# Kernel optimization log

Hardware: AMD Instinct MI355X
Metric: run time of the kernel (lower is better)

Reference implementation:

```python
import jax, jax.numpy as jnp
import numpy as np

B, K, S, L, H, A = 32, 128, 48, 2, 128, 500
NEG_INF = jnp.float32(-1e30)  # stand-in for -inf that is safe under fp16/bf16 too


def _gather_beam(x, idx):
    # x: (B, K, ...); idx: (B, K) -> x gathered along beam dim
    idx_b = idx.reshape(idx.shape + (1,) * (x.ndim - 2))
    return jnp.take_along_axis(x, jnp.broadcast_to(idx_b, idx.shape + x.shape[2:]), axis=1)


def setup_inputs() -> dict:
    key = jax.random.key(0)
    ks = jax.random.split(key, 12)
    return {
        "gen_ll": jax.random.normal(ks[0], (B, K), jnp.float32),
        "disc_ll": jax.random.normal(ks[1], (B, K), jnp.float32),
        "hiddens": jax.random.normal(ks[2], (B, K, S, L, H), jnp.float32),
        "cells": jax.random.normal(ks[3], (B, K, S, L, H), jnp.float32),
        "trees": jax.random.normal(ks[4], (B, K, S, H), jnp.float32),
        "beam_widths": jax.random.randint(ks[5], (B,), 1, K + 1, jnp.int64),
        "ncons_nts": jax.random.randint(ks[6], (B, K), 0, 8, jnp.int64),
        "nopen_parens": jax.random.randint(ks[7], (B, K), 0, 16, jnp.int64),
        "actions": jax.random.randint(ks[8], (B, K, A), 0, 30, jnp.int64),
        "actions_pos": jax.random.randint(ks[9], (B, K), 0, A, jnp.int64),
        "pointer": jax.random.randint(ks[10], (B, K), 0, S, jnp.int64),
        "size": 64,
    }


def reference(gen_ll, disc_ll, hiddens, cells, trees, beam_widths, ncons_nts,
              nopen_parens, actions, actions_pos, pointer, size):
    # BeamItems.shrink: mask beams outside active width, sort by score (desc),
    # gather all beam-indexed state by the sort permutation, clamp widths.
    beam_order = jnp.arange(K, dtype=beam_widths.dtype)          # (K,)
    outside = beam_order[None, :] >= beam_widths[:, None]        # (B, K)
    masked = jnp.where(outside, NEG_INF, gen_ll)                 # (B, K)

    sort_idx = jnp.argsort(-masked, axis=1)                      # descending
    gen_sorted = jnp.take_along_axis(masked, sort_idx, axis=1)

    disc_sorted = jnp.take_along_axis(disc_ll, sort_idx, axis=1)
    hiddens_s = _gather_beam(hiddens, sort_idx)
    cells_s = _gather_beam(cells, sort_idx)
    trees_s = _gather_beam(trees, sort_idx)
    ncons_s = jnp.take_along_axis(ncons_nts, sort_idx, axis=1)
    nopen_s = jnp.take_along_axis(nopen_parens, sort_idx, axis=1)
    actions_s = _gather_beam(actions, sort_idx)
    actions_pos_s = jnp.take_along_axis(actions_pos, sort_idx, axis=1)
    pointer_s = jnp.take_along_axis(pointer, sort_idx, axis=1)

    new_widths = jnp.minimum(beam_widths, jnp.asarray(size, beam_widths.dtype))
    return (gen_sorted, disc_sorted, hiddens_s, cells_s, trees_s,
            new_widths, ncons_s, nopen_s, actions_s, actions_pos_s, pointer_s)
```

## Files before the change

kernel.cpp:

```cpp
#include <hip/hip_runtime.h>

#define BB 32
#define KK 128
#define SS 48
#define LL 2
#define HH 128
#define AA 500

static constexpr float NEG_INF = -1e30f;

static constexpr long SZ_BK    = (long)BB * KK;
static constexpr long SZ_HID   = (long)BB * KK * SS * LL * HH;
static constexpr long SZ_TREE  = (long)BB * KK * SS * HH;
static constexpr long SZ_ACT   = (long)BB * KK * AA;

static constexpr long OFF_GEN   = 0;
static constexpr long OFF_DISC  = OFF_GEN  + SZ_BK;
static constexpr long OFF_HID   = OFF_DISC + SZ_BK;
static constexpr long OFF_CELL  = OFF_HID  + SZ_HID;
static constexpr long OFF_TREE  = OFF_CELL + SZ_HID;
static constexpr long OFF_WID   = OFF_TREE + SZ_TREE;
static constexpr long OFF_NCONS = OFF_WID  + BB;
static constexpr long OFF_NOPEN = OFF_NCONS + SZ_BK;
static constexpr long OFF_ACT   = OFF_NOPEN + SZ_BK;
static constexpr long OFF_APOS  = OFF_ACT  + SZ_ACT;
static constexpr long OFF_PTR   = OFF_APOS + SZ_BK;

__global__ void sort_small_kernel(
    const float* __restrict__ gen_ll,
    const float* __restrict__ disc_ll,
    const int*   __restrict__ beam_widths,
    const int*   __restrict__ ncons,
    const int*   __restrict__ nopen,
    const int*   __restrict__ actions_pos,
    const int*   __restrict__ pointer,
    const int*   __restrict__ size_ptr,
    float*       __restrict__ out,
    int*         __restrict__ perm_ws)
{
    const int b = blockIdx.x;
    const int i = threadIdx.x;

    __shared__ float mv[KK];
    __shared__ int   perm[KK];

    const int bw = beam_widths[b];
    float v = gen_ll[b * KK + i];
    if (i >= bw) v = NEG_INF;
    mv[i] = v;
    __syncthreads();

    int rank = 0;
#pragma unroll 8
    for (int j = 0; j < KK; ++j) {
        float vj = mv[j];
        rank += (vj > v) || (vj == v && j < i);
    }
    perm[rank] = i;
    __syncthreads();

    const int src = perm[i];
    perm_ws[b * KK + i] = src;

    out[OFF_GEN   + b * KK + i] = mv[src];
    out[OFF_DISC  + b * KK + i] = disc_ll[b * KK + src];
    out[OFF_NCONS + b * KK + i] = (float)ncons[b * KK + src];
    out[OFF_NOPEN + b * KK + i] = (float)nopen[b * KK + src];
    out[OFF_APOS  + b * KK + i] = (float)actions_pos[b * KK + src];
    out[OFF_PTR   + b * KK + i] = (float)pointer[b * KK + src];

    if (i == 0) {
        int sz = size_ptr[0];
        out[OFF_WID + b] = (float)(bw < sz ? bw : sz);
    }
}

__global__ void gather_f4(const float4* __restrict__ in,
                          float4*       __restrict__ out,
                          const int*    __restrict__ perm,
                          int inner4, int total4)
{
    int g = blockIdx.x * blockDim.x + threadIdx.x;
    if (g >= total4) return;
    int bk = g / inner4;
    int r  = g - bk * inner4;
    int b  = bk >> 7;
    int src = perm[bk];
    out[g] = in[(b * KK + src) * inner4 + r];
}

__global__ void gather_actions(const int4* __restrict__ in,
                               float4*     __restrict__ out,
                               const int*  __restrict__ perm)
{
    const int total4 = BB * KK * (AA / 4);
    int g = blockIdx.x * blockDim.x + threadIdx.x;
    if (g >= total4) return;
    const int inner4 = AA / 4;
    int bk = g / inner4;
    int r  = g - bk * inner4;
    int b  = bk >> 7;
    int src = perm[bk];
    int4 a = in[(b * KK + src) * inner4 + r];
    out[g] = make_float4((float)a.x, (float)a.y, (float)a.z, (float)a.w);
}

extern "C" void kernel_launch(void* const* d_in, const int* in_sizes, int n_in,
                              void* d_out, int out_size, void* d_ws, size_t ws_size,
                              hipStream_t stream) {
    const float* gen_ll      = (const float*)d_in[0];
    const float* disc_ll     = (const float*)d_in[1];
    const float* hiddens     = (const float*)d_in[2];
    const float* cells       = (const float*)d_in[3];
    const float* trees       = (const float*)d_in[4];
    const int*   beam_widths = (const int*)d_in[5];
    const int*   ncons       = (const int*)d_in[6];
    const int*   nopen       = (const int*)d_in[7];
    const int*   actions     = (const int*)d_in[8];
    const int*   actions_pos = (const int*)d_in[9];
    const int*   pointer     = (const int*)d_in[10];
    const int*   size_ptr    = (const int*)d_in[11];

    float* out = (float*)d_out;
    int*   perm_ws = (int*)d_ws;

    sort_small_kernel<<<BB, KK, 0, stream>>>(
        gen_ll, disc_ll, beam_widths, ncons, nopen, actions_pos, pointer,
        size_ptr, out, perm_ws);

    const int block = 256;

    {
        const int inner4 = SS * LL * HH / 4;
        const int total4 = (int)(SZ_HID / 4);
        gather_f4<<<(total4 + block - 1) / block, block, 0, stream>>>(
            (const float4*)hiddens, (float4*)(out + OFF_HID), perm_ws, inner4, total4);
    }
    {
        const int inner4 = SS * LL * HH / 4;
        const int total4 = (int)(SZ_HID / 4);
        gather_f4<<<(total4 + block - 1) / block, block, 0, stream>>>(
            (const float4*)cells, (float4*)(out + OFF_CELL), perm_ws, inner4, total4);
    }
    {
        const int inner4 = SS * HH / 4;
        const int total4 = (int)(SZ_TREE / 4);
        gather_f4<<<(total4 + block - 1) / block, block, 0, stream>>>(
            (const float4*)trees, (float4*)(out + OFF_TREE), perm_ws, inner4, total4);
    }
    {
        const int total4 = BB * KK * (AA / 4);
        gather_actions<<<(total4 + block - 1) / block, block, 0, stream>>>(
            (const int4*)actions, (float4*)(out + OFF_ACT), perm_ws);
    }
}
```

Baseline: 184.7 us.

## Fuse beam gathers into one 2D-grid kernel with nontemporal loads/stores

```diff
diff --git a/kernel.cpp b/kernel.cpp
--- a/kernel.cpp
+++ b/kernel.cpp
@@ -25,6 +25,9 @@
 static constexpr long OFF_ACT   = OFF_NOPEN + SZ_BK;
 static constexpr long OFF_APOS  = OFF_ACT  + SZ_ACT;
 static constexpr long OFF_PTR   = OFF_APOS + SZ_BK;
+
+typedef float f32x4 __attribute__((ext_vector_type(4)));
+typedef int   i32x4 __attribute__((ext_vector_type(4)));
 
 __global__ void sort_small_kernel(
     const float* __restrict__ gen_ll,
@@ -75,34 +78,43 @@
     }
 }
 
-__global__ void gather_f4(const float4* __restrict__ in,
-                          float4*       __restrict__ out,
-                          const int*    __restrict__ perm,
-                          int inner4, int total4)
+__global__ __launch_bounds__(256) void gather_fused(
+    const f32x4* __restrict__ hiddens,
+    const f32x4* __restrict__ cells,
+    const f32x4* __restrict__ trees,
+    const i32x4* __restrict__ actions,
+    const int*   __restrict__ perm,
+    float*       __restrict__ out)
 {
-    int g = blockIdx.x * blockDim.x + threadIdx.x;
-    if (g >= total4) return;
-    int bk = g / inner4;
-    int r  = g - bk * inner4;
-    int b  = bk >> 7;
-    int src = perm[bk];
-    out[g] = in[(b * KK + src) * inner4 + r];
-}
+    const int bk  = blockIdx.y;
+    const int c   = blockIdx.x;
+    const int tid = threadIdx.x;
+    const int b   = bk >> 7;
+    const int src = perm[bk];
+    const int srow = b * KK + src;
 
-__global__ void gather_actions(const int4* __restrict__ in,
-                               float4*     __restrict__ out,
-                               const int*  __restrict__ perm)
-{
-    const int total4 = BB * KK * (AA / 4);
-    int g = blockIdx.x * blockDim.x + threadIdx.x;
-    if (g >= total4) return;
-    const int inner4 = AA / 4;
-    int bk = g / inner4;
-    int r  = g - bk * inner4;
-    int b  = bk >> 7;
-    int src = perm[bk];
-    int4 a = in[(b * KK + src) * inner4 + r];
-    out[g] = make_float4((float)a.x, (float)a.y, (float)a.z, (float)a.w);
+    if (c < 24) {
+        const bool is_h = c < 12;
+        const int cc = is_h ? c : c - 12;
+        const f32x4* in = is_h ? hiddens : cells;
+        f32x4* o = (f32x4*)(out + (is_h ? OFF_HID : OFF_CELL));
+        const int r = cc * 256 + tid;
+        f32x4 v = __builtin_nontemporal_load(&in[(long)srow * 3072 + r]);
+        __builtin_nontemporal_store(v, &o[(long)bk * 3072 + r]);
+    } else if (c < 30) {
+        const int r = (c - 24) * 256 + tid;
+        f32x4 v = __builtin_nontemporal_load(&trees[(long)srow * 1536 + r]);
+        f32x4* o = (f32x4*)(out + OFF_TREE);
+        __builtin_nontemporal_store(v, &o[(long)bk * 1536 + r]);
+    } else {
+        if (tid < 125) {
+            i32x4 a = __builtin_nontemporal_load(&actions[(long)srow * 125 + tid]);
+            f32x4 v;
+            v.x = (float)a.x; v.y = (float)a.y; v.z = (float)a.z; v.w = (float)a.w;
+            f32x4* o = (f32x4*)(out + OFF_ACT);
+            __builtin_nontemporal_store(v, &o[(long)bk * 125 + tid]);
+        }
+    }
 }
 
 extern "C" void kernel_launch(void* const* d_in, const int* in_sizes, int n_in,
@@ -128,29 +140,8 @@
         gen_ll, disc_ll, beam_widths, ncons, nopen, actions_pos, pointer,
         size_ptr, out, perm_ws);
 
-    const int block = 256;
-
-    {
-        const int inner4 = SS * LL * HH / 4;
-        const int total4 = (int)(SZ_HID / 4);
-        gather_f4<<<(total4 + block - 1) / block, block, 0, stream>>>(
-            (const float4*)hiddens, (float4*)(out + OFF_HID), perm_ws, inner4, total4);
-    }
-    {
-        const int inner4 = SS * LL * HH / 4;
-        const int total4 = (int)(SZ_HID / 4);
-        gather_f4<<<(total4 + block - 1) / block, block, 0, stream>>>(
-            (const float4*)cells, (float4*)(out + OFF_CELL), perm_ws, inner4, total4);
-    }
-    {
-        const int inner4 = SS * HH / 4;
-        const int total4 = (int)(SZ_TREE / 4);
-        gather_f4<<<(total4 + block - 1) / block, block, 0, stream>>>(
-            (const float4*)trees, (float4*)(out + OFF_TREE), perm_ws, inner4, total4);
-    }
-    {
-        const int total4 = BB * KK * (AA / 4);
-        gather_actions<<<(total4 + block - 1) / block, block, 0, stream>>>(
-            (const int4*)actions, (float4*)(out + OFF_ACT), perm_ws);
-    }
+    dim3 grid(31, BB * KK);
+    gather_fused<<<grid, 256, 0, stream>>>(
+        (const f32x4*)hiddens, (const f32x4*)cells, (const f32x4*)trees,
+        (const i32x4*)actions, perm_ws, out);
 }
```

Measured after the change: 172.2 us, median of 2. 1.07x faster.
